# Performance work log

Hardware: AMD Instinct MI355X
Metric: run time of the kernel (lower is better)

## Reference

```python
import jax, jax.numpy as jnp
import numpy as np

B, S, D = 2, 2048, 1024
H = 16
HD = D // H  # head_dim = 64


def setup_inputs() -> dict:
    key = jax.random.key(0)
    ks = jax.random.split(key, 9)
    sc_in = 1.0 / np.sqrt(D)
    return {
        "x": jax.random.normal(ks[0], (B, S, D), dtype=jnp.float32),
        "Wq": jax.random.normal(ks[1], (D, D), dtype=jnp.float32) * sc_in,
        "bq": jnp.zeros((D,), dtype=jnp.float32),
        "Wk": jax.random.normal(ks[2], (D, D), dtype=jnp.float32) * sc_in,
        "bk": jnp.zeros((D,), dtype=jnp.float32),
        "Wv": jax.random.normal(ks[3], (D, D), dtype=jnp.float32) * sc_in,
        "bv": jnp.zeros((D,), dtype=jnp.float32),
        "Wo": jax.random.normal(ks[4], (D, D), dtype=jnp.float32) * sc_in,
        "bo": jnp.zeros((D,), dtype=jnp.float32),
    }


def reference(x, Wq, bq, Wk, bk, Wv, bv, Wo, bo):
    # QKV projections: [B,S,D] -> [B,H,S,HD]
    def split_heads(t):
        return t.reshape(B, S, H, HD).transpose(0, 2, 1, 3)

    Q = split_heads(x @ Wq + bq)
    K = split_heads(x @ Wk + bk)
    V = split_heads(x @ Wv + bv)

    scale = 1.0 / np.sqrt(HD).astype(np.float32)
    scores = jnp.einsum("bhqd,bhkd->bhqk", Q, K) * scale  # [B,H,S,S]
    weights = jax.nn.softmax(scores, axis=-1)
    # dropout(p=0.1) is identity in eval mode
    attended = jnp.einsum("bhqk,bhkd->bhqd", weights, V)  # [B,H,S,HD]
    attended = attended.transpose(0, 2, 1, 3).reshape(B, S, D)
    return attended @ Wo + bo
```

## Files before the change

### kernel.cpp

```cpp
#include <hip/hip_runtime.h>
#include <hip/hip_bf16.h>


#define S_ 2048
#define D_ 1024
#define HD_ 64
#define LDSW 72
#define QSZ 4194304

typedef __attribute__((ext_vector_type(8))) short bf16x8;
typedef __attribute__((ext_vector_type(4))) float f32x4;

static __device__ __forceinline__ short f2bs(float f) {
    __hip_bfloat16 h = __float2bfloat16(f);
    return *reinterpret_cast<short*>(&h);
}
static __device__ __forceinline__ float bs2f(short s) {
    __hip_bfloat16 h = *reinterpret_cast<__hip_bfloat16*>(&s);
    return __bfloat162float(h);
}
static __device__ __forceinline__ bf16x8 cvt8(const float* p) {
    f32x4 u0 = *(const f32x4*)p;
    f32x4 u1 = *(const f32x4*)(p + 4);
    bf16x8 r;
    r[0] = f2bs(u0[0]); r[1] = f2bs(u0[1]); r[2] = f2bs(u0[2]); r[3] = f2bs(u0[3]);
    r[4] = f2bs(u1[0]); r[5] = f2bs(u1[1]); r[6] = f2bs(u1[2]); r[7] = f2bs(u1[3]);
    return r;
}
static __device__ __forceinline__ void gld16(const void* g, void* l) {
    __builtin_amdgcn_global_load_lds(
        (const __attribute__((address_space(1))) unsigned int*)g,
        (__attribute__((address_space(3))) unsigned int*)l, 16, 0, 0);
}
static __device__ __forceinline__ int detect_f32(const unsigned int* __restrict__ xw) {
    const unsigned int w = xw[threadIdx.x & 63];
    const int e = (int)((w >> 7) & 0xFFu);
    unsigned long long m = __ballot(e >= 117 && e <= 130);
    return (__popcll(m) >= 32) ? 0 : 1;
}

__global__ __launch_bounds__(256) void prep(
    const void* __restrict__ x,
    const void* __restrict__ w0, const void* __restrict__ w1,
    const void* __restrict__ w2, const void* __restrict__ w3,
    short* __restrict__ Wt, short* __restrict__ Xb)
{
    __shared__ __align__(16) short Ts[64 * LDSW];
    const int f32in = detect_f32((const unsigned int*)x);
    const int idx = blockIdx.x;

    if (idx >= 1024) {
        const int c = idx - 1024;
        const size_t base = (size_t)c * 8192 + (size_t)threadIdx.x * 8;
        if (f32in) {
            const float* xf = (const float*)x;
            #pragma unroll
            for (int i = 0; i < 4; ++i)
                *(bf16x8*)&Xb[base + (size_t)i * 2048] = cvt8(xf + base + (size_t)i * 2048);
        } else {
            const short* xs = (const short*)x;
            #pragma unroll
            for (int i = 0; i < 4; ++i)
                *(bf16x8*)&Xb[base + (size_t)i * 2048] = *(const bf16x8*)(xs + base + (size_t)i * 2048);
        }
        return;
    }

    const int z = idx >> 8, bb = idx & 255;
    const void* W = z == 0 ? w0 : z == 1 ? w1 : z == 2 ? w2 : w3;
    short* O = Wt + (size_t)z * D_ * D_;
    const int k0 = (bb & 15) * 64, n0 = (bb >> 4) * 64;
    const int t = threadIdx.x;
    const int row = t >> 2, seg = t & 3;

    if (f32in) {
        const float* wg = (const float*)W + (size_t)(k0 + row) * D_ + n0;
        *(bf16x8*)&Ts[row * LDSW + seg * 8]      = cvt8(wg + seg * 8);
        *(bf16x8*)&Ts[row * LDSW + seg * 8 + 32] = cvt8(wg + seg * 8 + 32);
    } else {
        const short* wg = (const short*)W + (size_t)(k0 + row) * D_ + n0;
        *(bf16x8*)&Ts[row * LDSW + seg * 8]      = *(const bf16x8*)(wg + seg * 8);
        *(bf16x8*)&Ts[row * LDSW + seg * 8 + 32] = *(const bf16x8*)(wg + seg * 8 + 32);
    }
    __syncthreads();

    short* og = O + (size_t)(n0 + row) * D_ + k0;
    #pragma unroll
    for (int g = 0; g < 2; ++g) {
        const int ks = seg * 8 + g * 32;
        alignas(16) short tmp[8];
        #pragma unroll
        for (int i = 0; i < 8; ++i) tmp[i] = Ts[(ks + i) * LDSW + row];
        *(bf16x8*)(og + ks) = *(const bf16x8*)tmp;
    }
}

__global__ __launch_bounds__(256) void gemm_qkv(
    const short* __restrict__ Xb, const short* __restrict__ Wt3,
    const void* __restrict__ bq, const void* __restrict__ bk,
    const void* __restrict__ bv, short* __restrict__ out,
    const unsigned int* __restrict__ xw)
{
    __shared__ __align__(16) short As[128 * 64];
    __shared__ __align__(16) short Bs[128 * 64];
    const int ext_f32 = detect_f32(xw);
    const int t = threadIdx.x;
    const int wave = t >> 6, lane = t & 63;
    const int quad = lane >> 4, l16 = lane & 15;
    const int wm = wave & 1, wn = wave >> 1;
    const int m0 = blockIdx.x * 128, n0 = blockIdx.y * 128;
    const int id = n0 >> 10;
    const int lr = lane >> 3;
    const int kx = ((lane & 7) ^ (lr & 7)) * 8;

    f32x4 acc[4][4];
    #pragma unroll
    for (int i = 0; i < 4; ++i)
        #pragma unroll
        for (int j = 0; j < 4; ++j) acc[i][j] = (f32x4){0.f, 0.f, 0.f, 0.f};

    const size_t arow = (size_t)(m0 + wave * 32 + lr) * D_ + kx;
    const short* Bb = Wt3 + (size_t)(n0 + wave * 32 + lr) * D_ + kx;

    for (int kb = 0; kb < 16; ++kb) {
        __syncthreads();
        const int k0 = kb * 64;
        #pragma unroll
        for (int i = 0; i < 4; ++i)
            gld16(Xb + arow + (size_t)i * 8 * D_ + k0, &As[(wave * 4 + i) * 512]);
        #pragma unroll
        for (int i = 0; i < 4; ++i)
            gld16(Bb + (size_t)i * 8 * D_ + k0, &Bs[(wave * 4 + i) * 512]);
        __syncthreads();

        #pragma unroll
        for (int ks = 0; ks < 2; ++ks) {
            const int sw = ((ks * 4 + quad) ^ (l16 & 7)) * 8;
            bf16x8 af[4], bfr[4];
            #pragma unroll
            for (int i = 0; i < 4; ++i) {
                af[i]  = *(const bf16x8*)&As[(wm * 64 + i * 16 + l16) * 64 + sw];
                bfr[i] = *(const bf16x8*)&Bs[(wn * 64 + i * 16 + l16) * 64 + sw];
            }
            #pragma unroll
            for (int mi = 0; mi < 4; ++mi)
                #pragma unroll
                for (int ni = 0; ni < 4; ++ni)
                    acc[mi][ni] = __builtin_amdgcn_mfma_f32_16x16x32_bf16(
                        af[mi], bfr[ni], acc[mi][ni], 0, 0, 0);
        }
    }

    const void* bias = id == 0 ? bq : id == 1 ? bk : bv;
    const float oscale = id == 0 ? 0.18033688011112042f : 1.0f;
    #pragma unroll
    for (int ni = 0; ni < 4; ++ni) {
        const int n = n0 + wn * 64 + ni * 16 + l16;
        const int nl = n & 1023, h = nl >> 6, d = nl & 63;
        const float bvl = ext_f32 ? ((const float*)bias)[nl]
                                  : bs2f(((const short*)bias)[nl]);
        #pragma unroll
        for (int mi = 0; mi < 4; ++mi)
            #pragma unroll
            for (int r = 0; r < 4; ++r) {
                const int m = m0 + wm * 64 + mi * 16 + quad * 4 + r;
                const int b = m >> 11, s = m & 2047;
                const int bh = b * 16 + h;
                const float v = (acc[mi][ni][r] + bvl) * oscale;
                const size_t idx = (id < 2)
                    ? (size_t)id * QSZ + ((size_t)bh * S_ + s) * HD_ + d
                    : (size_t)2 * QSZ + ((size_t)bh * HD_ + d) * S_ + s;
                out[idx] = f2bs(v);
            }
    }
}

__global__ __launch_bounds__(256) void gemm_out(
    const short* __restrict__ A, const short* __restrict__ Bt,
    const void* __restrict__ bias, void* __restrict__ C,
    const unsigned int* __restrict__ xw)
{
    __shared__ __align__(16) short As[64 * 64];
    __shared__ __align__(16) short Bs[128 * 64];
    const int ext_f32 = detect_f32(xw);
    const int t = threadIdx.x;
    const int wave = t >> 6, lane = t & 63;
    const int quad = lane >> 4, l16 = lane & 15;
    const int wm = wave & 1, wn = wave >> 1;
    const int m0 = blockIdx.x * 64, n0 = blockIdx.y * 128;
    const int lr = lane >> 3;
    const int kx = ((lane & 7) ^ (lr & 7)) * 8;

    f32x4 acc[2][4];
    #pragma unroll
    for (int i = 0; i < 2; ++i)
        #pragma unroll
        for (int j = 0; j < 4; ++j) acc[i][j] = (f32x4){0.f, 0.f, 0.f, 0.f};

    const short* Ab = A  + (size_t)(m0 + wave * 16 + lr) * D_ + kx;
    const short* Bb = Bt + (size_t)(n0 + wave * 32 + lr) * D_ + kx;

    for (int kb = 0; kb < 16; ++kb) {
        __syncthreads();
        const int k0 = kb * 64;
        #pragma unroll
        for (int i = 0; i < 2; ++i)
            gld16(Ab + (size_t)i * 8 * D_ + k0, &As[(wave * 2 + i) * 512]);
        #pragma unroll
        for (int i = 0; i < 4; ++i)
            gld16(Bb + (size_t)i * 8 * D_ + k0, &Bs[(wave * 4 + i) * 512]);
        __syncthreads();

        #pragma unroll
        for (int ks = 0; ks < 2; ++ks) {
            const int sw = ((ks * 4 + quad) ^ (l16 & 7)) * 8;
            bf16x8 af[2], bfr[4];
            #pragma unroll
            for (int i = 0; i < 2; ++i)
                af[i] = *(const bf16x8*)&As[(wm * 32 + i * 16 + l16) * 64 + sw];
            #pragma unroll
            for (int i = 0; i < 4; ++i)
                bfr[i] = *(const bf16x8*)&Bs[(wn * 64 + i * 16 + l16) * 64 + sw];
            #pragma unroll
            for (int mi = 0; mi < 2; ++mi)
                #pragma unroll
                for (int ni = 0; ni < 4; ++ni)
                    acc[mi][ni] = __builtin_amdgcn_mfma_f32_16x16x32_bf16(
                        af[mi], bfr[ni], acc[mi][ni], 0, 0, 0);
        }
    }

    #pragma unroll
    for (int ni = 0; ni < 4; ++ni) {
        const int n = n0 + wn * 64 + ni * 16 + l16;
        const float bvl = ext_f32 ? ((const float*)bias)[n]
                                  : bs2f(((const short*)bias)[n]);
        #pragma unroll
        for (int mi = 0; mi < 2; ++mi)
            #pragma unroll
            for (int r = 0; r < 4; ++r) {
                const int m = m0 + wm * 32 + mi * 16 + quad * 4 + r;
                const float v = acc[mi][ni][r] + bvl;
                const size_t idx = (size_t)m * D_ + n;
                if (ext_f32) ((float*)C)[idx] = v;
                else         ((short*)C)[idx] = f2bs(v);
            }
    }
}

__global__ __launch_bounds__(512) void attn(
    const short* __restrict__ Q, const short* __restrict__ K,
    const short* __restrict__ Vt, short* __restrict__ Aout)
{
    __shared__ __align__(16) short Ks[2][64 * 64];
    __shared__ __align__(16) short Vs[2][64 * 64];
    __shared__ __align__(16) short Ps[8][16 * LDSW];

    const int t = threadIdx.x;
    const int wave = t >> 6, lane = t & 63;
    const int quad = lane >> 4, l16 = lane & 15;
    const int bh = blockIdx.x;
    const int q0 = blockIdx.y * 128;
    const int lr = lane >> 3;
    const int kx = ((lane & 7) ^ (lr & 7)) * 8;
    short* pw = &Ps[wave][0];

    bf16x8 bq0, bq1;
    {
        const short* qr = Q + ((size_t)bh * S_ + q0 + wave * 16 + l16) * HD_ + quad * 8;
        bq0 = *(const bf16x8*)qr;
        bq1 = *(const bf16x8*)(qr + 32);
    }

    bf16x8 ones;
    #pragma unroll
    for (int i = 0; i < 8; ++i) ones[i] = (short)0x3F80;

    f32x4 o[4], lacc;
    lacc = (f32x4){0.f, 0.f, 0.f, 0.f};
    #pragma unroll
    for (int nt = 0; nt < 4; ++nt) o[nt] = (f32x4){0.f, 0.f, 0.f, 0.f};

    const short* Kb = K  + ((size_t)bh * S_  + wave * 8 + lr) * HD_ + kx;
    const short* Vb = Vt + ((size_t)bh * HD_ + wave * 8 + lr) * S_ + kx;

    gld16(Kb, &Ks[0][wave * 512]);
    gld16(Vb, &Vs[0][wave * 512]);
    __syncthreads();

    for (int j = 0; j < 32; ++j) {
        const int cur = j & 1;
        if (j < 31) {
            gld16(Kb + (size_t)((j + 1) * 64) * HD_, &Ks[cur ^ 1][wave * 512]);
            gld16(Vb + (j + 1) * 64,                 &Vs[cur ^ 1][wave * 512]);
        }

        f32x4 st[4];
        #pragma unroll
        for (int nt = 0; nt < 4; ++nt) {
            bf16x8 kf0 = *(const bf16x8*)&Ks[cur][(nt * 16 + l16) * 64 + ((quad ^ (l16 & 7)) * 8)];
            bf16x8 kf1 = *(const bf16x8*)&Ks[cur][(nt * 16 + l16) * 64 + (((4 + quad) ^ (l16 & 7)) * 8)];
            f32x4 z = (f32x4){0.f, 0.f, 0.f, 0.f};
            z = __builtin_amdgcn_mfma_f32_16x16x32_bf16(kf0, bq0, z, 0, 0, 0);
            z = __builtin_amdgcn_mfma_f32_16x16x32_bf16(kf1, bq1, z, 0, 0, 0);
            st[nt] = z;
        }

        #pragma unroll
        for (int nt = 0; nt < 4; ++nt) {
            unsigned u0 = __float_as_uint(__builtin_amdgcn_exp2f(st[nt][0]));
            unsigned u1 = __float_as_uint(__builtin_amdgcn_exp2f(st[nt][1]));
            unsigned u2 = __float_as_uint(__builtin_amdgcn_exp2f(st[nt][2]));
            unsigned u3 = __float_as_uint(__builtin_amdgcn_exp2f(st[nt][3]));
            uint2 pk;
            pk.x = __builtin_amdgcn_perm(u1, u0, 0x07060302);
            pk.y = __builtin_amdgcn_perm(u3, u2, 0x07060302);
            *(uint2*)&pw[l16 * LDSW + nt * 16 + quad * 4] = pk;
        }
        __builtin_amdgcn_s_waitcnt(0xc07f);

        #pragma unroll
        for (int ks = 0; ks < 2; ++ks) {
            bf16x8 vf[4];
            #pragma unroll
            for (int nt = 0; nt < 4; ++nt)
                vf[nt] = *(const bf16x8*)&Vs[cur][(nt * 16 + l16) * 64 + (((ks * 4 + quad) ^ (l16 & 7)) * 8)];
            bf16x8 ap = *(const bf16x8*)&pw[l16 * LDSW + ks * 32 + quad * 8];
            lacc = __builtin_amdgcn_mfma_f32_16x16x32_bf16(ap, ones, lacc, 0, 0, 0);
            #pragma unroll
            for (int nt = 0; nt < 4; ++nt)
                o[nt] = __builtin_amdgcn_mfma_f32_16x16x32_bf16(ap, vf[nt], o[nt], 0, 0, 0);
        }

        __syncthreads();
    }

    const int b = bh >> 4, h = bh & 15;
    #pragma unroll
    for (int r = 0; r < 4; ++r) {
        const float inv = 1.f / lacc[r];
        const int s = q0 + wave * 16 + quad * 4 + r;
        const size_t base = ((size_t)b * S_ + s) * D_ + h * HD_;
        #pragma unroll
        for (int nt = 0; nt < 4; ++nt)
            Aout[base + nt * 16 + l16] = f2bs(o[nt][r] * inv);
    }
}

extern "C" void kernel_launch(void* const* d_in, const int* in_sizes, int n_in,
                              void* d_out, int out_size, void* d_ws, size_t ws_size,
                              hipStream_t stream) {
    char* ws = (char*)d_ws;
    short* Wt  = (short*)(ws + ((size_t)1  << 20));
    short* Att = (short*)(ws + ((size_t)9  << 20));
    short* Xb  = Att;
    short* QKV = (short*)(ws + ((size_t)17 << 20));
    const unsigned int* xw = (const unsigned int*)d_in[0];

    prep<<<1536, 256, 0, stream>>>(d_in[0], d_in[1], d_in[3], d_in[5], d_in[7], Wt, Xb);
    gemm_qkv<<<dim3(32, 24), 256, 0, stream>>>(Xb, Wt, d_in[2], d_in[4], d_in[6], QKV, xw);
    attn<<<dim3(32, 16), 512, 0, stream>>>(QKV, QKV + QSZ, QKV + 2 * QSZ, Att);
    gemm_out<<<dim3(64, 8), 256, 0, stream>>>(Att, Wt + (3 << 20), d_in[8], d_out, xw);
}
```

Before: 197.2 us.

## Double-buffer LDS tiles in QKV and output projection GEMMs

Both projection GEMMs now keep two LDS buffers per operand. The next K-slice is prefetched with direct global-to-LDS loads while MFMAs run on the current slice, and the loop needs only one barrier per iteration instead of two. This is meant to hide global load latency behind compute. In exchange it doubles LDS use (64 KB for the QKV kernel), which may lower occupancy. It also relies on gld16 completing before the barrier, which depends on how gld16 waits (vmcnt).

```diff
diff --git a/kernel.cpp b/kernel.cpp
--- a/kernel.cpp
+++ b/kernel.cpp
@@ -101,8 +101,8 @@
     const void* __restrict__ bv, short* __restrict__ out,
     const unsigned int* __restrict__ xw)
 {
-    __shared__ __align__(16) short As[128 * 64];
-    __shared__ __align__(16) short Bs[128 * 64];
+    __shared__ __align__(16) short As[2][128 * 64];
+    __shared__ __align__(16) short Bs[2][128 * 64];
     const int ext_f32 = detect_f32(xw);
     const int t = threadIdx.x;
     const int wave = t >> 6, lane = t & 63;
@@ -119,19 +119,26 @@
         #pragma unroll
         for (int j = 0; j < 4; ++j) acc[i][j] = (f32x4){0.f, 0.f, 0.f, 0.f};
 
-    const size_t arow = (size_t)(m0 + wave * 32 + lr) * D_ + kx;
+    const short* Ab = Xb  + (size_t)(m0 + wave * 32 + lr) * D_ + kx;
     const short* Bb = Wt3 + (size_t)(n0 + wave * 32 + lr) * D_ + kx;
 
+    #pragma unroll
+    for (int i = 0; i < 4; ++i) {
+        gld16(Ab + (size_t)i * 8 * D_, &As[0][(wave * 4 + i) * 512]);
+        gld16(Bb + (size_t)i * 8 * D_, &Bs[0][(wave * 4 + i) * 512]);
+    }
+    __syncthreads();
+
     for (int kb = 0; kb < 16; ++kb) {
-        __syncthreads();
-        const int k0 = kb * 64;
-        #pragma unroll
-        for (int i = 0; i < 4; ++i)
-            gld16(Xb + arow + (size_t)i * 8 * D_ + k0, &As[(wave * 4 + i) * 512]);
-        #pragma unroll
-        for (int i = 0; i < 4; ++i)
-            gld16(Bb + (size_t)i * 8 * D_ + k0, &Bs[(wave * 4 + i) * 512]);
-        __syncthreads();
+        const int cur = kb & 1;
+        if (kb < 15) {
+            const int kn = (kb + 1) * 64;
+            #pragma unroll
+            for (int i = 0; i < 4; ++i) {
+                gld16(Ab + (size_t)i * 8 * D_ + kn, &As[cur ^ 1][(wave * 4 + i) * 512]);
+                gld16(Bb + (size_t)i * 8 * D_ + kn, &Bs[cur ^ 1][(wave * 4 + i) * 512]);
+            }
+        }
 
         #pragma unroll
         for (int ks = 0; ks < 2; ++ks) {
@@ -139,8 +146,8 @@
             bf16x8 af[4], bfr[4];
             #pragma unroll
             for (int i = 0; i < 4; ++i) {
-                af[i]  = *(const bf16x8*)&As[(wm * 64 + i * 16 + l16) * 64 + sw];
-                bfr[i] = *(const bf16x8*)&Bs[(wn * 64 + i * 16 + l16) * 64 + sw];
+                af[i]  = *(const bf16x8*)&As[cur][(wm * 64 + i * 16 + l16) * 64 + sw];
+                bfr[i] = *(const bf16x8*)&Bs[cur][(wn * 64 + i * 16 + l16) * 64 + sw];
             }
             #pragma unroll
             for (int mi = 0; mi < 4; ++mi)
@@ -149,6 +156,8 @@
                     acc[mi][ni] = __builtin_amdgcn_mfma_f32_16x16x32_bf16(
                         af[mi], bfr[ni], acc[mi][ni], 0, 0, 0);
         }
+
+        __syncthreads();
     }
 
     const void* bias = id == 0 ? bq : id == 1 ? bk : bv;
@@ -180,8 +189,8 @@
     const void* __restrict__ bias, void* __restrict__ C,
     const unsigned int* __restrict__ xw)
 {
-    __shared__ __align__(16) short As[64 * 64];
-    __shared__ __align__(16) short Bs[128 * 64];
+    __shared__ __align__(16) short As[2][64 * 64];
+    __shared__ __align__(16) short Bs[2][128 * 64];
     const int ext_f32 = detect_f32(xw);
     const int t = threadIdx.x;
     const int wave = t >> 6, lane = t & 63;
@@ -200,16 +209,25 @@
     const short* Ab = A  + (size_t)(m0 + wave * 16 + lr) * D_ + kx;
     const short* Bb = Bt + (size_t)(n0 + wave * 32 + lr) * D_ + kx;
 
+    #pragma unroll
+    for (int i = 0; i < 2; ++i)
+        gld16(Ab + (size_t)i * 8 * D_, &As[0][(wave * 2 + i) * 512]);
+    #pragma unroll
+    for (int i = 0; i < 4; ++i)
+        gld16(Bb + (size_t)i * 8 * D_, &Bs[0][(wave * 4 + i) * 512]);
+    __syncthreads();
+
     for (int kb = 0; kb < 16; ++kb) {
-        __syncthreads();
-        const int k0 = kb * 64;
-        #pragma unroll
-        for (int i = 0; i < 2; ++i)
-            gld16(Ab + (size_t)i * 8 * D_ + k0, &As[(wave * 2 + i) * 512]);
-        #pragma unroll
-        for (int i = 0; i < 4; ++i)
-            gld16(Bb + (size_t)i * 8 * D_ + k0, &Bs[(wave * 4 + i) * 512]);
-        __syncthreads();
+        const int cur = kb & 1;
+        if (kb < 15) {
+            const int kn = (kb + 1) * 64;
+            #pragma unroll
+            for (int i = 0; i < 2; ++i)
+                gld16(Ab + (size_t)i * 8 * D_ + kn, &As[cur ^ 1][(wave * 2 + i) * 512]);
+            #pragma unroll
+            for (int i = 0; i < 4; ++i)
+                gld16(Bb + (size_t)i * 8 * D_ + kn, &Bs[cur ^ 1][(wave * 4 + i) * 512]);
+        }
 
         #pragma unroll
         for (int ks = 0; ks < 2; ++ks) {
@@ -217,10 +235,10 @@
             bf16x8 af[2], bfr[4];
             #pragma unroll
             for (int i = 0; i < 2; ++i)
-                af[i] = *(const bf16x8*)&As[(wm * 32 + i * 16 + l16) * 64 + sw];
+                af[i] = *(const bf16x8*)&As[cur][(wm * 32 + i * 16 + l16) * 64 + sw];
             #pragma unroll
             for (int i = 0; i < 4; ++i)
-                bfr[i] = *(const bf16x8*)&Bs[(wn * 64 + i * 16 + l16) * 64 + sw];
+                bfr[i] = *(const bf16x8*)&Bs[cur][(wn * 64 + i * 16 + l16) * 64 + sw];
             #pragma unroll
             for (int mi = 0; mi < 2; ++mi)
                 #pragma unroll
@@ -228,6 +246,8 @@
                     acc[mi][ni] = __builtin_amdgcn_mfma_f32_16x16x32_bf16(
                         af[mi], bfr[ni], acc[mi][ni], 0, 0, 0);
         }
+
+        __syncthreads();
     }
 
     #pragma unroll
```

Result: slower. 202.5 us (+2.7%).
